# Kernel tuning notes

Measured on AMD Instinct MI355X. Metric: run time of the kernel, lower is better.

The kernel has to match this reference:

```python
import jax, jax.numpy as jnp
import numpy as np

B, NX, NY = 4, 16384, 16384
CX = CY = 256
CK = CV = 256
H = 8


def setup_inputs() -> dict:
    key = jax.random.key(0)
    ks = jax.random.split(key, 12)
    s = 0.02
    return {
        "x": jax.random.normal(ks[0], (B, NX, CX), jnp.float32),
        "y": jax.random.normal(ks[1], (B, NY, CY), jnp.float32),
        "x_pos_embed": jax.random.normal(ks[2], (B, NX, CX), jnp.float32),
        "y_pos_embed": jax.random.normal(ks[3], (B, NY, CY), jnp.float32),
        "Wq": jax.random.normal(ks[4], (CK, CX), jnp.float32) * s,
        "bq": jnp.zeros((CK,), jnp.float32),
        "Wk": jax.random.normal(ks[5], (CK, CY), jnp.float32) * s,
        "bk": jnp.zeros((CK,), jnp.float32),
        "Wv": jax.random.normal(ks[6], (CV, CY), jnp.float32) * s,
        "bv": jnp.zeros((CV,), jnp.float32),
        "Wr": jax.random.normal(ks[7], (CX, CV), jnp.float32) * s,
        "br": jnp.zeros((CX,), jnp.float32),
    }


def reference(x, y, x_pos_embed, y_pos_embed, Wq, bq, Wk, bk, Wv, bv, Wr, br):
    # Linear projections (nn.Linear: x @ W.T + b)
    q = (x + x_pos_embed) @ Wq.T + bq            # [B, Nx, Ck]
    k = (y + y_pos_embed) @ Wk.T + bk            # [B, Ny, Ck]
    v = y @ Wv.T + bv                            # [B, Ny, Cv]

    dk, dv = CK // H, CV // H
    # Split heads: [B, N, H, d] -> [B, H, N, d]
    q = q.reshape(B, NX, H, dk).transpose(0, 2, 1, 3)
    k = k.reshape(B, NY, H, dk).transpose(0, 2, 1, 3)
    v = v.reshape(B, NY, H, dv).transpose(0, 2, 1, 3)

    # key softmax over tokens (Ny); query softmax over per-head channels (dk)
    k = jax.nn.softmax(k, axis=2)                # [B, H, Ny, dk]
    q = jax.nn.softmax(q, axis=3)                # [B, H, Nx, dk]

    # context = softmax(K)^T V : [B, H, dk, dv]
    context = jnp.einsum('bhnk,bhnv->bhkv', k, v)
    # attended = Q context : [B, H, Nx, dv]
    attended = jnp.einsum('bhnk,bhkv->bhnv', q, context)

    # merge heads -> [B, Nx, Cv], reproject -> [B, Nx, Cx]
    agg = attended.transpose(0, 2, 1, 3).reshape(B, NX, CV)
    return agg @ Wr.T + br
```

## Files before the change

### kernel.cpp

```cpp
#include <hip/hip_runtime.h>


typedef float f32x4 __attribute__((ext_vector_type(4)));
typedef short s16x4 __attribute__((ext_vector_type(4)));
typedef short s16x8 __attribute__((ext_vector_type(8)));

#define MFMA16(A, B, C) __builtin_amdgcn_mfma_f32_16x16x32_bf16((A), (B), (C), 0, 0, 0)

__device__ __forceinline__ short f2bf(float f) {
    unsigned u = __builtin_bit_cast(unsigned, f);
    u = (u + 0x7FFFu + ((u >> 16) & 1u)) >> 16;
    return (short)u;
}
__device__ __forceinline__ float bf2f(short b) {
    unsigned u = ((unsigned)(unsigned short)b) << 16;
    return __builtin_bit_cast(float, u);
}
__device__ __forceinline__ f32x4 ntld4f(const float* p) {
    return __builtin_nontemporal_load((const f32x4*)p);
}
__device__ __forceinline__ s16x8 ntld8s(const short* p) {
    return __builtin_nontemporal_load((const s16x8*)p);
}
__device__ __forceinline__ void ntst8s(short* p, s16x8 v) {
    __builtin_nontemporal_store(v, (s16x8*)p);
}
__device__ __forceinline__ void ntst4f(float* p, f32x4 v) {
    __builtin_nontemporal_store(v, (f32x4*)p);
}

__global__ __launch_bounds__(256) void wcvt_kernel(
    const float* __restrict__ wq, const float* __restrict__ wk,
    const float* __restrict__ wv, const float* __restrict__ wr,
    short* __restrict__ wbf)
{
    int id = blockIdx.x * 256 + threadIdx.x;
    int m = id >> 13;
    int slot = id & 8191;
    int tile = slot >> 9;
    int ks   = (slot >> 6) & 7;
    int lane = slot & 63;
    int lrow = lane & 15, lgrp = lane >> 4;
    const float* src = (m == 0) ? wq : (m == 1) ? wk : (m == 2) ? wv : wr;
    const float* p = src + (size_t)(tile * 16 + lrow) * 256 + ks * 32 + lgrp * 8;
    f32x4 a = *(const f32x4*)p;
    f32x4 b = *(const f32x4*)(p + 4);
    s16x8 o;
    o[0]=f2bf(a[0]); o[1]=f2bf(a[1]); o[2]=f2bf(a[2]); o[3]=f2bf(a[3]);
    o[4]=f2bf(b[0]); o[5]=f2bf(b[1]); o[6]=f2bf(b[2]); o[7]=f2bf(b[3]);
    *(s16x8*)(wbf + (size_t)id * 8) = o;
}

__global__ __launch_bounds__(256, 4) void kv_kernel(
    const float* __restrict__ y, const float* __restrict__ ypos,
    const short* __restrict__ wkp, const short* __restrict__ wvp,
    const float* __restrict__ bk, const float* __restrict__ bv,
    short* __restrict__ e_buf, short* __restrict__ v_buf)
{
    __shared__ short smem[32 * 512];
    short* ak = smem;
    short* av = smem + 32 * 256;
    const int row0 = blockIdx.x * 32;
    const int t = threadIdx.x;
    const int w = t >> 6, lane = t & 63;

    {
        #pragma unroll
        for (int it = 0; it < 8; ++it) {
            int r = it * 4 + w;
            f32x4 a = ntld4f(y    + (size_t)(row0 + r) * 256 + lane * 4);
            f32x4 p = ntld4f(ypos + (size_t)(row0 + r) * 256 + lane * 4);
            f32x4 k = a + p;
            s16x4 ov, ok;
            ov[0]=f2bf(a[0]); ov[1]=f2bf(a[1]); ov[2]=f2bf(a[2]); ov[3]=f2bf(a[3]);
            ok[0]=f2bf(k[0]); ok[1]=f2bf(k[1]); ok[2]=f2bf(k[2]); ok[3]=f2bf(k[3]);
            int swz = ((lane >> 1) ^ (r & 7)) * 8 + (lane & 1) * 4;
            *(s16x4*)(av + r * 256 + swz) = ov;
            *(s16x4*)(ak + r * 256 + swz) = ok;
        }
    }
    __syncthreads();

    const int lrow = lane & 15, lgrp = lane >> 4;
    const bool is_k = (w < 2);
    const int colbase = (w & 1) * 128;
    const int tile0 = colbase >> 4;
    const short* WP = is_k ? wkp : wvp;
    const float* bp = is_k ? bk : bv;
    const short* A = is_k ? ak : av;

    float bias[8];
    #pragma unroll
    for (int nf = 0; nf < 8; ++nf) bias[nf] = bp[colbase + nf * 16 + lrow];

    s16x8 af[2][8];
    #pragma unroll
    for (int mf = 0; mf < 2; ++mf) {
        int rr = mf * 16 + lrow;
        #pragma unroll
        for (int ks = 0; ks < 8; ++ks) {
            int cs = ((ks * 4 + lgrp) ^ (rr & 7));
            af[mf][ks] = *(const s16x8*)(A + rr * 256 + cs * 8);
        }
    }
    __syncthreads();

    #pragma unroll
    for (int nf = 0; nf < 8; ++nf) {
        const int tile = tile0 + nf;
        const short* wt = WP + ((size_t)tile * 8) * 512 + lane * 8;
        f32x4 a0 = (f32x4){0.f, 0.f, 0.f, 0.f};
        f32x4 a1 = (f32x4){0.f, 0.f, 0.f, 0.f};
        #pragma unroll
        for (int kg = 0; kg < 2; ++kg) {
            s16x8 bf[4];
            #pragma unroll
            for (int kk = 0; kk < 4; ++kk)
                bf[kk] = *(const s16x8*)(wt + (kg * 4 + kk) * 512);
            #pragma unroll
            for (int kk = 0; kk < 4; ++kk) {
                a0 = MFMA16(af[0][kg * 4 + kk], bf[kk], a0);
                a1 = MFMA16(af[1][kg * 4 + kk], bf[kk], a1);
            }
        }
        const int colp = (is_k ? 0 : 256) + colbase + nf * 16 + lrow;
        #pragma unroll
        for (int rr = 0; rr < 4; ++rr) {
            float v0 = a0[rr] + bias[nf];
            float v1 = a1[rr] + bias[nf];
            if (is_k) { v0 = __expf(v0); v1 = __expf(v1); }
            int lr0 = lgrp * 4 + rr;
            int lr1 = lr0 + 16;
            smem[lr0 * 512 + (((colp >> 3) ^ (lr0 & 7)) * 8) + (colp & 7)] = f2bf(v0);
            smem[lr1 * 512 + (((colp >> 3) ^ (lr1 & 7)) * 8) + (colp & 7)] = f2bf(v1);
        }
    }
    __syncthreads();

    {
        #pragma unroll
        for (int i = 0; i < 8; ++i) {
            int r = i * 4 + w;
            int grow = row0 + r;
            s16x8 val = *(const s16x8*)(smem + r * 512 + ((lane ^ (r & 7)) << 3));
            if (lane < 32)
                ntst8s(e_buf + (size_t)grow * 256 + lane * 8, val);
            else
                ntst8s(v_buf + (size_t)grow * 256 + (lane - 32) * 8, val);
        }
    }
}

__global__ __launch_bounds__(256) void ctx_kernel(
    const short* __restrict__ e_buf, const short* __restrict__ v_buf,
    float* __restrict__ partials)
{
    __shared__ float se[128 * 32];
    __shared__ float sv[128 * 32];
    __shared__ float red[4 * 1056];
    const int cb = blockIdx.x, bh = blockIdx.y;
    const int b = bh >> 3, h = bh & 7;
    const int tok0 = b * 16384 + cb * 1024;
    const int t = threadIdx.x, w = t >> 6, lane = t & 63;
    const int ckb = (lane >> 3) * 4, cvb = (lane & 7) * 4;

    f32x4 acc[4];
    #pragma unroll
    for (int i = 0; i < 4; ++i) acc[i] = (f32x4){0.f, 0.f, 0.f, 0.f};
    f32x4 dn = (f32x4){0.f, 0.f, 0.f, 0.f};

    for (int it = 0; it < 8; ++it) {
        __syncthreads();
        #pragma unroll
        for (int s = 0; s < 2; ++s) {
            int id = t + s * 256;
            int rr = id >> 2, pp = id & 3;
            size_t g = (size_t)(tok0 + it * 128 + rr) * 256 + h * 32 + pp * 8;
            s16x8 ee = ntld8s(e_buf + g);
            s16x8 vv = ntld8s(v_buf + g);
            f32x4 e0 = {bf2f(ee[0]), bf2f(ee[1]), bf2f(ee[2]), bf2f(ee[3])};
            f32x4 e1 = {bf2f(ee[4]), bf2f(ee[5]), bf2f(ee[6]), bf2f(ee[7])};
            f32x4 v0 = {bf2f(vv[0]), bf2f(vv[1]), bf2f(vv[2]), bf2f(vv[3])};
            f32x4 v1 = {bf2f(vv[4]), bf2f(vv[5]), bf2f(vv[6]), bf2f(vv[7])};
            *(f32x4*)(se + rr * 32 + pp * 8)     = e0;
            *(f32x4*)(se + rr * 32 + pp * 8 + 4) = e1;
            *(f32x4*)(sv + rr * 32 + pp * 8)     = v0;
            *(f32x4*)(sv + rr * 32 + pp * 8 + 4) = v1;
        }
        __syncthreads();
        const int r0 = w * 32;
        #pragma unroll 8
        for (int rr = 0; rr < 32; ++rr) {
            f32x4 e4 = *(const f32x4*)(se + (r0 + rr) * 32 + ckb);
            f32x4 v4 = *(const f32x4*)(sv + (r0 + rr) * 32 + cvb);
            acc[0] += e4[0] * v4;
            acc[1] += e4[1] * v4;
            acc[2] += e4[2] * v4;
            acc[3] += e4[3] * v4;
            dn += e4;
        }
    }
    __syncthreads();
    #pragma unroll
    for (int i = 0; i < 4; ++i)
        *(f32x4*)(red + w * 1056 + (ckb + i) * 32 + cvb) = acc[i];
    if ((lane & 7) == 0)
        *(f32x4*)(red + w * 1056 + 1024 + ckb) = dn;
    __syncthreads();
    float* outp = partials + (size_t)(bh * 16 + cb) * 1056;
    for (int e = t; e < 1056; e += 256)
        outp[e] = red[e] + red[1056 + e] + red[2112 + e] + red[3168 + e];
}

__global__ __launch_bounds__(256) void ctx_reduce_kernel(
    const float* __restrict__ partials, short* __restrict__ ctxT)
{
    __shared__ float s[1056];
    const int bh = blockIdx.x, t = threadIdx.x;
    for (int e = t; e < 1056; e += 256) {
        float a = 0.f;
        for (int c = 0; c < 16; ++c) a += partials[(size_t)(bh * 16 + c) * 1056 + e];
        s[e] = a;
    }
    __syncthreads();
    for (int e = t; e < 1024; e += 256) {
        int ck = e >> 5, cv = e & 31;
        float val = s[e] / s[1024 + ck];
        ctxT[(size_t)bh * 1024 + cv * 32 + ck] = f2bf(val);
    }
}

__global__ __launch_bounds__(256) void qout_kernel(
    const float* __restrict__ x, const float* __restrict__ xpos,
    const short* __restrict__ wqp, const float* __restrict__ bq,
    const short* __restrict__ ctxT,
    const short* __restrict__ wrp, const float* __restrict__ br,
    float* __restrict__ out)
{
    __shared__ short smem[32 * 512];
    short* alds = smem;
    const int row0 = blockIdx.x * 32;
    const int b = row0 >> 14;
    const int t = threadIdx.x;
    const int w = t >> 6, lane = t & 63;

    {
        f32x4 lx[8], lp[8];
        #pragma unroll
        for (int it = 0; it < 8; ++it) {
            int r = it * 4 + w;
            lx[it] = ntld4f(x    + (size_t)(row0 + r) * 256 + lane * 4);
            lp[it] = ntld4f(xpos + (size_t)(row0 + r) * 256 + lane * 4);
        }
        #pragma unroll
        for (int it = 0; it < 8; ++it) {
            int r = it * 4 + w;
            f32x4 a = lx[it] + lp[it];
            s16x4 o;
            o[0]=f2bf(a[0]); o[1]=f2bf(a[1]); o[2]=f2bf(a[2]); o[3]=f2bf(a[3]);
            int swz = ((lane >> 1) ^ (r & 7)) * 8 + (lane & 1) * 4;
            *(s16x4*)(alds + r * 256 + swz) = o;
        }
    }
    __syncthreads();

    const int lrow = lane & 15, lgrp = lane >> 4;
    const int wc = w * 64;
    const int tile0 = wc >> 4;

    float biasq[4];
    #pragma unroll
    for (int nf = 0; nf < 4; ++nf) biasq[nf] = bq[wc + nf * 16 + lrow];

    f32x4 acc[2][4];
    #pragma unroll
    for (int mf = 0; mf < 2; ++mf)
        #pragma unroll
        for (int nf = 0; nf < 4; ++nf) acc[mf][nf] = (f32x4){0.f, 0.f, 0.f, 0.f};

    {
        const short* wq8 = wqp + lane * 8;
        s16x8 bfq[2][4];
        #pragma unroll
        for (int nf = 0; nf < 4; ++nf)
            bfq[0][nf] = *(const s16x8*)(wq8 + ((size_t)(tile0 + nf) * 8 + 0) * 512);
        #pragma unroll
        for (int ks = 0; ks < 8; ++ks) {
            const int cur = ks & 1, nxt = cur ^ 1;
            if (ks < 7) {
                #pragma unroll
                for (int nf = 0; nf < 4; ++nf)
                    bfq[nxt][nf] = *(const s16x8*)(wq8 + ((size_t)(tile0 + nf) * 8 + ks + 1) * 512);
            }
            s16x8 af[2];
            #pragma unroll
            for (int mf = 0; mf < 2; ++mf) {
                int rr = mf * 16 + lrow;
                int cs = (ks * 4 + lgrp) ^ (rr & 7);
                af[mf] = *(const s16x8*)(alds + rr * 256 + cs * 8);
            }
            #pragma unroll
            for (int nf = 0; nf < 4; ++nf) {
                acc[0][nf] = MFMA16(af[0], bfq[cur][nf], acc[0][nf]);
                acc[1][nf] = MFMA16(af[1], bfq[cur][nf], acc[1][nf]);
            }
        }
    }

    short* ql = smem + 8192 + w * 2048;
    #pragma unroll
    for (int mf = 0; mf < 2; ++mf) {
        f32x4 e[4];
        #pragma unroll
        for (int nf = 0; nf < 4; ++nf)
            #pragma unroll
            for (int rr = 0; rr < 4; ++rr)
                e[nf][rr] = __expf(acc[mf][nf][rr] + biasq[nf]);
        #pragma unroll
        for (int hl = 0; hl < 2; ++hl) {
            #pragma unroll
            for (int rr = 0; rr < 4; ++rr) {
                float s = e[hl * 2][rr] + e[hl * 2 + 1][rr];
                s += __shfl_xor(s, 1);
                s += __shfl_xor(s, 2);
                s += __shfl_xor(s, 4);
                s += __shfl_xor(s, 8);
                float rinv = 1.0f / s;
                int row = mf * 16 + lgrp * 4 + rr;
                #pragma unroll
                for (int n2 = 0; n2 < 2; ++n2) {
                    int colc = hl * 32 + n2 * 16 + lrow;
                    int cs = (colc >> 3) ^ (row & 7);
                    ql[row * 64 + cs * 8 + (colc & 7)] = f2bf(e[hl * 2 + n2][rr] * rinv);
                }
            }
        }
    }
    __syncthreads();

    f32x4 att[2][2][2];
    #pragma unroll
    for (int hl = 0; hl < 2; ++hl)
        #pragma unroll
        for (int mf = 0; mf < 2; ++mf)
            #pragma unroll
            for (int n2 = 0; n2 < 2; ++n2) att[hl][mf][n2] = (f32x4){0.f,0.f,0.f,0.f};

    #pragma unroll
    for (int hl = 0; hl < 2; ++hl) {
        const short* cbase = ctxT + (size_t)(b * 8 + w * 2 + hl) * 1024;
        s16x8 bctx[2];
        #pragma unroll
        for (int n2 = 0; n2 < 2; ++n2)
            bctx[n2] = *(const s16x8*)(cbase + (n2 * 16 + lrow) * 32 + lgrp * 8);
        #pragma unroll
        for (int mf = 0; mf < 2; ++mf) {
            int row = mf * 16 + lrow;
            int cs = (hl * 4 + lgrp) ^ (row & 7);
            s16x8 aq = *(const s16x8*)(ql + row * 64 + cs * 8);
            #pragma unroll
            for (int n2 = 0; n2 < 2; ++n2)
                att[hl][mf][n2] = MFMA16(aq, bctx[n2], att[hl][mf][n2]);
        }
    }

    #pragma unroll
    for (int hl = 0; hl < 2; ++hl)
      #pragma unroll
      for (int mf = 0; mf < 2; ++mf)
        #pragma unroll
        for (int n2 = 0; n2 < 2; ++n2)
          #pragma unroll
          for (int rr = 0; rr < 4; ++rr) {
              int row = mf * 16 + lgrp * 4 + rr;
              int col = wc + hl * 32 + n2 * 16 + lrow;
              int cs = (col >> 3) ^ (row & 7);
              alds[row * 256 + cs * 8 + (col & 7)] = f2bf(att[hl][mf][n2][rr]);
          }
    __syncthreads();

    float biasr[4];
    #pragma unroll
    for (int nf = 0; nf < 4; ++nf) biasr[nf] = br[wc + nf * 16 + lrow];

    f32x4 acc2[2][4];
    #pragma unroll
    for (int mf = 0; mf < 2; ++mf)
        #pragma unroll
        for (int nf = 0; nf < 4; ++nf) acc2[mf][nf] = (f32x4){0.f, 0.f, 0.f, 0.f};

    {
        const short* wr8 = wrp + lane * 8;
        s16x8 bfr[2][4];
        #pragma unroll
        for (int nf = 0; nf < 4; ++nf)
            bfr[0][nf] = *(const s16x8*)(wr8 + ((size_t)(tile0 + nf) * 8 + 0) * 512);
        #pragma unroll
        for (int ks = 0; ks < 8; ++ks) {
            const int cur = ks & 1, nxt = cur ^ 1;
            if (ks < 7) {
                #pragma unroll
                for (int nf = 0; nf < 4; ++nf)
                    bfr[nxt][nf] = *(const s16x8*)(wr8 + ((size_t)(tile0 + nf) * 8 + ks + 1) * 512);
            }
            s16x8 af[2];
            #pragma unroll
            for (int mf = 0; mf < 2; ++mf) {
                int rr = mf * 16 + lrow;
                int cs = (ks * 4 + lgrp) ^ (rr & 7);
                af[mf] = *(const s16x8*)(alds + rr * 256 + cs * 8);
            }
            #pragma unroll
            for (int nf = 0; nf < 4; ++nf) {
                acc2[0][nf] = MFMA16(af[0], bfr[cur][nf], acc2[0][nf]);
                acc2[1][nf] = MFMA16(af[1], bfr[cur][nf], acc2[1][nf]);
            }
        }
    }
    __syncthreads();

    float* cf = (float*)smem;
    #pragma unroll
    for (int mf = 0; mf < 2; ++mf)
      #pragma unroll
      for (int nf = 0; nf < 4; ++nf)
        #pragma unroll
        for (int rr = 0; rr < 4; ++rr) {
            int row = mf * 16 + lgrp * 4 + rr;
            int col = wc + nf * 16 + lrow;
            int chunk = col >> 2, pos = col & 3;
            cf[row * 256 + ((chunk ^ (row & 7)) << 2) + pos] = acc2[mf][nf][rr] + biasr[nf];
        }
    __syncthreads();

    #pragma unroll
    for (int i = 0; i < 8; ++i) {
        int r = i * 4 + w;
        f32x4 val = *(const f32x4*)(cf + r * 256 + (((lane ^ (r & 7)) & 63) << 2));
        ntst4f(out + (size_t)(row0 + r) * 256 + lane * 4, val);
    }
}

extern "C" void kernel_launch(void* const* d_in, const int* in_sizes, int n_in,
                              void* d_out, int out_size, void* d_ws, size_t ws_size,
                              hipStream_t stream)
{
    const float* x    = (const float*)d_in[0];
    const float* y    = (const float*)d_in[1];
    const float* xpos = (const float*)d_in[2];
    const float* ypos = (const float*)d_in[3];
    const float* Wq   = (const float*)d_in[4];
    const float* bq   = (const float*)d_in[5];
    const float* Wk   = (const float*)d_in[6];
    const float* bk   = (const float*)d_in[7];
    const float* Wv   = (const float*)d_in[8];
    const float* bv   = (const float*)d_in[9];
    const float* Wr   = (const float*)d_in[10];
    const float* br   = (const float*)d_in[11];

    char*  ws    = (char*)d_ws;
    short* wbf   = (short*)(ws);
    short* ctxT  = (short*)(ws + 524288);
    float* parts = (float*)(ws + (1 << 20));
    short* e_buf = (short*)(ws + ((size_t)4 << 20));
    short* v_buf = e_buf + (size_t)65536 * 256;
    float* outp  = (float*)d_out;

    hipLaunchKernelGGL(wcvt_kernel, dim3(128), dim3(256), 0, stream,
                       Wq, Wk, Wv, Wr, wbf);
    hipLaunchKernelGGL(kv_kernel, dim3(2048), dim3(256), 0, stream,
                       y, ypos, wbf + 65536, wbf + 131072, bk, bv, e_buf, v_buf);
    hipLaunchKernelGGL(ctx_kernel, dim3(16, 32), dim3(256), 0, stream,
                       e_buf, v_buf, parts);
    hipLaunchKernelGGL(ctx_reduce_kernel, dim3(32), dim3(256), 0, stream,
                       parts, ctxT);
    hipLaunchKernelGGL(qout_kernel, dim3(2048), dim3(256), 0, stream,
                       x, xpos, wbf, bq, ctxT, wbf + 196608, br, outp);
}
```

Baseline: 158.7 us.

## Fold per-head context into output projection weights per batch

Precomputes M = blockdiag(context) · Wr^T per batch in the context-reduce kernel, so the query kernel goes straight from softmaxed Q to the output GEMM. This removes the per-tile attended MFMA stage, its LDS round trip and one barrier from the hot 2048-block kernel. In exchange, the small 32-block reduce kernel now does a scalar fp32 dot-product GEMM, and each batch reads its own bf16 M matrix instead of a shared Wr. It also replaces the manual bf16 rounding with the native __bf16 conversion.

```diff
diff --git a/kernel.cpp b/kernel.cpp
--- a/kernel.cpp
+++ b/kernel.cpp
@@ -8,9 +8,8 @@
 #define MFMA16(A, B, C) __builtin_amdgcn_mfma_f32_16x16x32_bf16((A), (B), (C), 0, 0, 0)
 
 __device__ __forceinline__ short f2bf(float f) {
-    unsigned u = __builtin_bit_cast(unsigned, f);
-    u = (u + 0x7FFFu + ((u >> 16) & 1u)) >> 16;
-    return (short)u;
+    __bf16 h = (__bf16)f;
+    return __builtin_bit_cast(short, h);
 }
 __device__ __forceinline__ float bf2f(short b) {
     unsigned u = ((unsigned)(unsigned short)b) << 16;
@@ -212,29 +211,47 @@
         outp[e] = red[e] + red[1056 + e] + red[2112 + e] + red[3168 + e];
 }
 
-__global__ __launch_bounds__(256) void ctx_reduce_kernel(
-    const float* __restrict__ partials, short* __restrict__ ctxT)
+__global__ __launch_bounds__(256) void ctxred2_kernel(
+    const float* __restrict__ partials, const float* __restrict__ wr,
+    short* __restrict__ mpk)
 {
     __shared__ float s[1056];
     const int bh = blockIdx.x, t = threadIdx.x;
+    const int b = bh >> 3, h = bh & 7;
     for (int e = t; e < 1056; e += 256) {
         float a = 0.f;
         for (int c = 0; c < 16; ++c) a += partials[(size_t)(bh * 16 + c) * 1056 + e];
         s[e] = a;
     }
     __syncthreads();
-    for (int e = t; e < 1024; e += 256) {
-        int ck = e >> 5, cv = e & 31;
-        float val = s[e] / s[1024 + ck];
-        ctxT[(size_t)bh * 1024 + cv * 32 + ck] = f2bf(val);
+    for (int e = t; e < 1024; e += 256)
+        s[e] = s[e] / s[1024 + (e >> 5)];
+    __syncthreads();
+
+    #pragma unroll 4
+    for (int i = 0; i < 32; ++i) {
+        int linear = i * 256 + t;
+        int tile = linear >> 9, rem = linear & 511;
+        int lane = rem >> 3, j = rem & 7;
+        int col = tile * 16 + (lane & 15);
+        int ck = (lane >> 4) * 8 + j;
+        const float* wrow = wr + (size_t)col * 256 + h * 32;
+        const float* cr = s + ck * 32;
+        float m = 0.f;
+        #pragma unroll
+        for (int dv = 0; dv < 32; dv += 4) {
+            f32x4 wv = *(const f32x4*)(wrow + dv);
+            m += cr[dv] * wv[0] + cr[dv + 1] * wv[1]
+               + cr[dv + 2] * wv[2] + cr[dv + 3] * wv[3];
+        }
+        mpk[(((size_t)(b * 16 + tile)) * 8 + h) * 512 + rem] = f2bf(m);
     }
 }
 
 __global__ __launch_bounds__(256) void qout_kernel(
     const float* __restrict__ x, const float* __restrict__ xpos,
     const short* __restrict__ wqp, const float* __restrict__ bq,
-    const short* __restrict__ ctxT,
-    const short* __restrict__ wrp, const float* __restrict__ br,
+    const short* __restrict__ mpk, const float* __restrict__ br,
     float* __restrict__ out)
 {
     __shared__ short smem[32 * 512];
@@ -306,8 +323,8 @@
             }
         }
     }
-
-    short* ql = smem + 8192 + w * 2048;
+    __syncthreads();
+
     #pragma unroll
     for (int mf = 0; mf < 2; ++mf) {
         f32x4 e[4];
@@ -329,56 +346,15 @@
                 int row = mf * 16 + lgrp * 4 + rr;
                 #pragma unroll
                 for (int n2 = 0; n2 < 2; ++n2) {
-                    int colc = hl * 32 + n2 * 16 + lrow;
-                    int cs = (colc >> 3) ^ (row & 7);
-                    ql[row * 64 + cs * 8 + (colc & 7)] = f2bf(e[hl * 2 + n2][rr] * rinv);
+                    int col = wc + hl * 32 + n2 * 16 + lrow;
+                    int cs = (col >> 3) ^ (row & 7);
+                    alds[row * 256 + cs * 8 + (col & 7)] = f2bf(e[hl * 2 + n2][rr] * rinv);
                 }
             }
         }
     }
     __syncthreads();
 
-    f32x4 att[2][2][2];
-    #pragma unroll
-    for (int hl = 0; hl < 2; ++hl)
-        #pragma unroll
-        for (int mf = 0; mf < 2; ++mf)
-            #pragma unroll
-            for (int n2 = 0; n2 < 2; ++n2) att[hl][mf][n2] = (f32x4){0.f,0.f,0.f,0.f};
-
-    #pragma unroll
-    for (int hl = 0; hl < 2; ++hl) {
-        const short* cbase = ctxT + (size_t)(b * 8 + w * 2 + hl) * 1024;
-        s16x8 bctx[2];
-        #pragma unroll
-        for (int n2 = 0; n2 < 2; ++n2)
-            bctx[n2] = *(const s16x8*)(cbase + (n2 * 16 + lrow) * 32 + lgrp * 8);
-        #pragma unroll
-        for (int mf = 0; mf < 2; ++mf) {
-            int row = mf * 16 + lrow;
-            int cs = (hl * 4 + lgrp) ^ (row & 7);
-            s16x8 aq = *(const s16x8*)(ql + row * 64 + cs * 8);
-            #pragma unroll
-            for (int n2 = 0; n2 < 2; ++n2)
-                att[hl][mf][n2] = MFMA16(aq, bctx[n2], att[hl][mf][n2]);
-        }
-    }
-
-    #pragma unroll
-    for (int hl = 0; hl < 2; ++hl)
-      #pragma unroll
-      for (int mf = 0; mf < 2; ++mf)
-        #pragma unroll
-        for (int n2 = 0; n2 < 2; ++n2)
-          #pragma unroll
-          for (int rr = 0; rr < 4; ++rr) {
-              int row = mf * 16 + lgrp * 4 + rr;
-              int col = wc + hl * 32 + n2 * 16 + lrow;
-              int cs = (col >> 3) ^ (row & 7);
-              alds[row * 256 + cs * 8 + (col & 7)] = f2bf(att[hl][mf][n2][rr]);
-          }
-    __syncthreads();
-
     float biasr[4];
     #pragma unroll
     for (int nf = 0; nf < 4; ++nf) biasr[nf] = br[wc + nf * 16 + lrow];
@@ -390,18 +366,18 @@
         for (int nf = 0; nf < 4; ++nf) acc2[mf][nf] = (f32x4){0.f, 0.f, 0.f, 0.f};
 
     {
-        const short* wr8 = wrp + lane * 8;
+        const short* mp8 = mpk + (size_t)b * 65536 + lane * 8;
         s16x8 bfr[2][4];
         #pragma unroll
         for (int nf = 0; nf < 4; ++nf)
-            bfr[0][nf] = *(const s16x8*)(wr8 + ((size_t)(tile0 + nf) * 8 + 0) * 512);
+            bfr[0][nf] = *(const s16x8*)(mp8 + ((size_t)(tile0 + nf) * 8 + 0) * 512);
         #pragma unroll
         for (int ks = 0; ks < 8; ++ks) {
             const int cur = ks & 1, nxt = cur ^ 1;
             if (ks < 7) {
                 #pragma unroll
                 for (int nf = 0; nf < 4; ++nf)
-                    bfr[nxt][nf] = *(const s16x8*)(wr8 + ((size_t)(tile0 + nf) * 8 + ks + 1) * 512);
+                    bfr[nxt][nf] = *(const s16x8*)(mp8 + ((size_t)(tile0 + nf) * 8 + ks + 1) * 512);
             }
             s16x8 af[2];
             #pragma unroll
@@ -460,7 +436,7 @@
 
     char*  ws    = (char*)d_ws;
     short* wbf   = (short*)(ws);
-    short* ctxT  = (short*)(ws + 524288);
+    short* mpk   = (short*)(ws + 524288);
     float* parts = (float*)(ws + (1 << 20));
     short* e_buf = (short*)(ws + ((size_t)4 << 20));
     short* v_buf = e_buf + (size_t)65536 * 256;
@@ -472,8 +448,8 @@
                        y, ypos, wbf + 65536, wbf + 131072, bk, bv, e_buf, v_buf);
     hipLaunchKernelGGL(ctx_kernel, dim3(16, 32), dim3(256), 0, stream,
                        e_buf, v_buf, parts);
-    hipLaunchKernelGGL(ctx_reduce_kernel, dim3(32), dim3(256), 0, stream,
-                       parts, ctxT);
+    hipLaunchKernelGGL(ctxred2_kernel, dim3(32), dim3(256), 0, stream,
+                       parts, Wr, mpk);
     hipLaunchKernelGGL(qout_kernel, dim3(2048), dim3(256), 0, stream,
-                       x, xpos, wbf, bq, ctxT, wbf + 196608, br, outp);
-}
+                       x, xpos, wbf, bq, mpk, br, outp);
+}
```

Result: slower. 168.4 us (+6.1%).
